# Performance work log

Measured on AMD Instinct MI355X. Metric: run time of the kernel, lower is better.

## Reference

```python
import jax, jax.numpy as jnp
import numpy as np

N_NODES = 50000
N_EDGES = 1600000
F_IN = 256
HID = 256
HEADS = 8
HD = HID // HEADS  # 32
SLOPE = 0.2
EPS = 1e-5


def setup_inputs() -> dict:
    key = jax.random.key(0)
    ks = jax.random.split(key, 10)
    node_features = jax.random.normal(ks[0], (N_NODES, F_IN), jnp.float32)
    edge_index = jax.random.randint(ks[1], (2, N_EDGES), 0, N_NODES, jnp.int32)
    s = 1.0 / np.sqrt(F_IN)
    W = jax.random.uniform(ks[2], (HEADS, F_IN, HD), jnp.float32, -s, s)
    bw = jax.random.uniform(ks[3], (HEADS, HD), jnp.float32, -s, s)
    sa = 1.0 / np.sqrt(2 * HD)
    A = jax.random.uniform(ks[4], (HEADS, 2 * HD), jnp.float32, -sa, sa)
    ba = jax.random.uniform(ks[5], (HEADS,), jnp.float32, -sa, sa)
    gamma = jnp.ones((HEADS, HD), jnp.float32)
    beta = jnp.zeros((HEADS, HD), jnp.float32)
    so = 1.0 / np.sqrt(HD)
    Wout = jax.random.uniform(ks[6], (HD, HID), jnp.float32, -so, so)
    bout = jax.random.uniform(ks[7], (HID,), jnp.float32, -so, so)
    return dict(node_features=node_features, edge_index=edge_index, W=W, bw=bw,
                A=A, ba=ba, gamma=gamma, beta=beta, Wout=Wout, bout=bout)


def _head(x, W, bw, a, ba, gamma, beta, tgt, src):
    h = x @ W + bw                         # [N, d]
    # attn(concat(h_i, h_j)) = h_i @ a1 + h_j @ a2 + ba  (linear over concat)
    si = h @ a[:HD]                        # [N]
    sj = h @ a[HD:]                        # [N]
    e = si[tgt] + sj[src] + ba             # [E]
    e = jnp.where(e >= 0, e, SLOPE * e)    # leaky_relu
    # scatter_softmax over edges grouped by target node (stable)
    m = jax.ops.segment_max(e, tgt, num_segments=N_NODES)
    ex = jnp.exp(e - m[tgt])
    den = jax.ops.segment_sum(ex, tgt, num_segments=N_NODES)
    alpha = ex / den[tgt]                  # [E]  (dropout in eval mode = identity)
    msg = alpha[:, None] * h[src]          # [E, d]
    agg = jax.ops.segment_sum(msg, tgt, num_segments=N_NODES)  # [N, d]
    out = agg + h                          # skip connection
    out = jnp.where(out > 0, out, jnp.expm1(out))  # ELU
    mu = out.mean(axis=-1, keepdims=True)
    var = out.var(axis=-1, keepdims=True)
    return (out - mu) * jax.lax.rsqrt(var + EPS) * gamma + beta


def reference(node_features, edge_index, W, bw, A, ba, gamma, beta, Wout, bout):
    tgt = edge_index[0]
    src = edge_index[1]
    heads = jax.vmap(_head, in_axes=(None, 0, 0, 0, 0, 0, 0, None, None))(
        node_features, W, bw, A, ba, gamma, beta, tgt, src)   # [H, N, d]
    mean = heads.mean(axis=0)                                  # [N, d]
    y = mean @ Wout + bout                                     # [N, HID]
    return jnp.where(y > 0, y, jnp.expm1(y))                   # ELU
```

## Files before the change

kernel.cpp:

```cpp
#include <hip/hip_runtime.h>
#include <hip/hip_bf16.h>

#define N_NODES 50000
#define N_EDGES 1600000
#define HEADS 8
#define HD 32
#define FIN 256
#define HID 256

typedef unsigned short u16;
typedef unsigned int u32;

typedef short s8v __attribute__((ext_vector_type(8)));
typedef float f4v __attribute__((ext_vector_type(4)));

__device__ __forceinline__ float bf2f(u16 v) {
  union { u32 u; float f; } c; c.u = ((u32)v) << 16; return c.f;
}
__device__ __forceinline__ u16 f2bf(float f) {
  union { u32 u; float f; } c; c.f = f;
  u32 u = c.u;
  return (u16)((u + 0x7FFFu + ((u >> 16) & 1u)) >> 16);
}
__device__ __forceinline__ u32 pk2(float lo, float hi) {
  return (u32)f2bf(lo) | ((u32)f2bf(hi) << 16);
}

__global__ __launch_bounds__(256) void k_gemm(
    const float* __restrict__ X, const float* __restrict__ W,
    const float* __restrict__ bw, const float* __restrict__ A,
    u16* __restrict__ Hb, float* __restrict__ si, float* __restrict__ sj) {
  __shared__ __align__(16) u16 Xs[128 * 40];
  __shared__ __align__(16) u16 Wt[128 * 40];

  const int t = threadIdx.x;
  const int m0 = (blockIdx.x >> 1) * 128;
  const int n0 = (blockIdx.x & 1) * 128;
  const int w = t >> 6;
  const int lane = t & 63;
  const int l15 = lane & 15;
  const int quad = lane >> 4;
  const int wm = (w >> 1) * 64;
  const int wn = (w & 1) * 64;

  f4v acc[4][4];
#pragma unroll
  for (int i = 0; i < 4; i++)
#pragma unroll
    for (int j = 0; j < 4; j++) acc[i][j] = (f4v){0.f, 0.f, 0.f, 0.f};

  const int nl = t & 127;
  const int half = t >> 7;
  const int gn = n0 + nl;
  const int gh = gn >> 5, gd = gn & 31;

  for (int k0 = 0; k0 < FIN; k0 += 32) {
#pragma unroll
    for (int p = 0; p < 4; p++) {
      int row = p * 32 + (t >> 3);
      int f4 = t & 7;
      int node = m0 + row;
      float4 xv = make_float4(0.f, 0.f, 0.f, 0.f);
      if (node < N_NODES) xv = *(const float4*)&X[node * FIN + k0 + f4 * 4];
      u32* dst = (u32*)&Xs[row * 40 + f4 * 4];
      dst[0] = pk2(xv.x, xv.y);
      dst[1] = pk2(xv.z, xv.w);
    }
    {
      const float* wp = W + gh * (FIN * HD) + (k0 + half * 16) * HD + gd;
#pragma unroll
      for (int j = 0; j < 8; j++) {
        float lo = wp[(2 * j) * HD];
        float hi = wp[(2 * j + 1) * HD];
        *(u32*)&Wt[nl * 40 + half * 16 + 2 * j] = pk2(lo, hi);
      }
    }
    __syncthreads();
    s8v af[4], bf[4];
#pragma unroll
    for (int mi = 0; mi < 4; mi++)
      af[mi] = *(const s8v*)&Xs[(wm + mi * 16 + l15) * 40 + quad * 8];
#pragma unroll
    for (int ni = 0; ni < 4; ni++)
      bf[ni] = *(const s8v*)&Wt[(wn + ni * 16 + l15) * 40 + quad * 8];
#pragma unroll
    for (int mi = 0; mi < 4; mi++)
#pragma unroll
      for (int ni = 0; ni < 4; ni++)
        acc[mi][ni] = __builtin_amdgcn_mfma_f32_16x16x32_bf16(af[mi], bf[ni], acc[mi][ni], 0, 0, 0);
    __syncthreads();
  }

  const int head0 = (n0 + wn) >> 5;
  const int head1 = head0 + 1;
  float c1a0 = A[head0 * 64 + l15],      c1a1 = A[head0 * 64 + 16 + l15];
  float c2a0 = A[head0 * 64 + 32 + l15], c2a1 = A[head0 * 64 + 48 + l15];
  float c1b0 = A[head1 * 64 + l15],      c1b1 = A[head1 * 64 + 16 + l15];
  float c2b0 = A[head1 * 64 + 32 + l15], c2b1 = A[head1 * 64 + 48 + l15];

#pragma unroll
  for (int mi = 0; mi < 4; mi++) {
#pragma unroll
    for (int ni = 0; ni < 4; ni++) {
      float b = bw[n0 + wn + ni * 16 + l15];
#pragma unroll
      for (int r = 0; r < 4; r++) acc[mi][ni][r] += b;
    }
    const int rbase = m0 + wm + mi * 16 + quad * 4;
#pragma unroll
    for (int r = 0; r < 4; r++) {
      int node = rbase + r;
      if (node < N_NODES) {
#pragma unroll
        for (int ni = 0; ni < 4; ni++) {
          int col = n0 + wn + ni * 16 + l15;
          Hb[node * HID + col] = f2bf(acc[mi][ni][r]);
        }
      }
    }
    float s1a[4], s2a[4], s1b[4], s2b[4];
#pragma unroll
    for (int r = 0; r < 4; r++) {
      s1a[r] = acc[mi][0][r] * c1a0 + acc[mi][1][r] * c1a1;
      s2a[r] = acc[mi][0][r] * c2a0 + acc[mi][1][r] * c2a1;
      s1b[r] = acc[mi][2][r] * c1b0 + acc[mi][3][r] * c1b1;
      s2b[r] = acc[mi][2][r] * c2b0 + acc[mi][3][r] * c2b1;
    }
#pragma unroll
    for (int off = 1; off <= 8; off <<= 1) {
#pragma unroll
      for (int r = 0; r < 4; r++) {
        s1a[r] += __shfl_xor(s1a[r], off);
        s2a[r] += __shfl_xor(s2a[r], off);
        s1b[r] += __shfl_xor(s1b[r], off);
        s2b[r] += __shfl_xor(s2b[r], off);
      }
    }
    if (l15 == 0) {
#pragma unroll
      for (int r = 0; r < 4; r++) {
        int node = rbase + r;
        if (node < N_NODES) {
          si[node * HEADS + head0] = s1a[r];
          sj[node * HEADS + head0] = s2a[r];
          si[node * HEADS + head1] = s1b[r];
          sj[node * HEADS + head1] = s2b[r];
        }
      }
    }
  }
}

__global__ void k_hist(const int* __restrict__ tgt, int* __restrict__ cnt) {
  int e = blockIdx.x * 256 + threadIdx.x;
  if (e < N_EDGES) atomicAdd(&cnt[tgt[e]], 1);
}

__global__ __launch_bounds__(256) void k_scan1(const int* __restrict__ cnt,
    int* __restrict__ excl, int* __restrict__ bsum) {
  __shared__ int s[256];
  const int t = threadIdx.x;
  const int i = blockIdx.x * 256 + t;
  int v = (i < N_NODES) ? cnt[i] : 0;
  s[t] = v;
  __syncthreads();
  int x = v;
  for (int off = 1; off < 256; off <<= 1) {
    int y = (t >= off) ? s[t - off] : 0;
    __syncthreads();
    x += y;
    s[t] = x;
    __syncthreads();
  }
  if (i < N_NODES) excl[i] = x - v;
  if (t == 255) bsum[blockIdx.x] = x;
}

__global__ __launch_bounds__(256) void k_scan2(const int* __restrict__ bsum,
                                               int* __restrict__ boff) {
  __shared__ int s[256];
  const int t = threadIdx.x;
  int v = (t < 196) ? bsum[t] : 0;
  s[t] = v;
  __syncthreads();
  int x = v;
  for (int off = 1; off < 256; off <<= 1) {
    int y = (t >= off) ? s[t - off] : 0;
    __syncthreads();
    x += y;
    s[t] = x;
    __syncthreads();
  }
  if (t < 196) boff[t] = x - v;
}

__global__ void k_scan3(const int* __restrict__ excl, const int* __restrict__ boff,
                        int* __restrict__ rowptr, int* __restrict__ cursor) {
  int i = blockIdx.x * 256 + threadIdx.x;
  if (i < N_NODES) {
    int v = excl[i] + boff[blockIdx.x];
    rowptr[i] = v;
    cursor[i] = v;
  }
}

__global__ void k_scatter(const int* __restrict__ tgt, const int* __restrict__ src,
                          int* __restrict__ cursor, int* __restrict__ sortedSrc) {
  int e = blockIdx.x * 256 + threadIdx.x;
  if (e < N_EDGES) {
    int tg = tgt[e];
    int pos = atomicAdd(&cursor[tg], 1);
    sortedSrc[pos] = src[e];
  }
}

__global__ __launch_bounds__(256) void k_fused(
    const u16* __restrict__ Hb, const float* __restrict__ si,
    const float* __restrict__ sj, const float* __restrict__ ba,
    const float* __restrict__ gamma, const float* __restrict__ beta,
    const float* __restrict__ Wout, const float* __restrict__ bout,
    const int* __restrict__ rowptr, const int* __restrict__ cnt,
    const int* __restrict__ sortedSrc, float* __restrict__ out) {
  __shared__ float exs[32 * 8];
  __shared__ u32   soff[32];
  __shared__ float sbase[8];
  __shared__ float accs[8][256];
  __shared__ float dens[8][32];
  __shared__ float lnorm[256];
  __shared__ float meanv[32];

  const int n = blockIdx.x;
  const int t = threadIdx.x;
  const int cg = t & 31;
  const int es = t >> 5;
  const int hh = cg >> 2;
  const int start = rowptr[n];
  const int deg = cnt[n];
  if (t < 8) sbase[t] = si[n * HEADS + t] + ba[t];
  __syncthreads();

  const int i2c = t >> 3, h8 = t & 7;
  float acc[8] = {0.f, 0.f, 0.f, 0.f, 0.f, 0.f, 0.f, 0.f};
  float den = 0.f;
  for (int base = 0; base < deg; base += 32) {
    const int m = min(32, deg - base);
    {
      float exv = 0.f;
      u32 off0 = 0;
      if (i2c < m) {
        int s = sortedSrc[start + base + i2c];
        float e = sbase[h8] + sj[s * HEADS + h8];
        e = (e >= 0.f) ? e : 0.2f * e;
        exv = __expf(e);
        off0 = (u32)s * (HID * 2);
      }
      exs[i2c * 8 + h8] = exv;
      if (h8 == 0) soff[i2c] = off0;
    }
    __syncthreads();
#pragma unroll
    for (int k = 0; k < 4; k++) {
      int i2 = k * 8 + es;
      u32 off = soff[i2];
      float exv = exs[i2 * 8 + hh];
      float4 hb4 = *(const float4*)((const char*)Hb + off + 16 * cg);
      const u32* hw = (const u32*)&hb4;
#pragma unroll
      for (int d = 0; d < 4; d++) {
        union { u32 u; float f; } lo, hi;
        lo.u = hw[d] << 16;
        hi.u = hw[d] & 0xFFFF0000u;
        acc[2 * d]     += exv * lo.f;
        acc[2 * d + 1] += exv * hi.f;
      }
      den += exv;
    }
    __syncthreads();
  }
#pragma unroll
  for (int j = 0; j < 8; j++) accs[es][cg * 8 + j] = acc[j];
  dens[es][cg] = den;
  __syncthreads();

  float accT = 0.f, denT = 0.f;
#pragma unroll
  for (int e2 = 0; e2 < 8; e2++) {
    accT += accs[e2][t];
    denT += dens[e2][t >> 3];
  }
  float hs = bf2f(Hb[n * HID + t]);
  float v = ((deg > 0) ? (accT / denT) : 0.f) + hs;
  v = (v > 0.f) ? v : expm1f(v);
  float sum = v, sq = v * v;
#pragma unroll
  for (int off = 16; off >= 1; off >>= 1) {
    sum += __shfl_xor(sum, off);
    sq  += __shfl_xor(sq, off);
  }
  float mu = sum * (1.f / 32.f);
  float var = sq * (1.f / 32.f) - mu * mu;
  float nv = (v - mu) * rsqrtf(var + 1e-5f) * gamma[t] + beta[t];
  lnorm[t] = nv;
  __syncthreads();
  if (t < 32) {
    float m2 = 0.f;
#pragma unroll
    for (int h2 = 0; h2 < HEADS; h2++) m2 += lnorm[h2 * 32 + t];
    meanv[t] = m2 * 0.125f;
  }
  __syncthreads();
  float y = bout[t];
#pragma unroll
  for (int k = 0; k < 32; k++) y += meanv[k] * Wout[k * HID + t];
  y = (y > 0.f) ? y : expm1f(y);
  out[n * HID + t] = y;
}

extern "C" void kernel_launch(void* const* d_in, const int* in_sizes, int n_in,
                              void* d_out, int out_size, void* d_ws, size_t ws_size,
                              hipStream_t stream) {
  const float* X     = (const float*)d_in[0];
  const int*   EI    = (const int*)d_in[1];
  const float* W     = (const float*)d_in[2];
  const float* bw    = (const float*)d_in[3];
  const float* A     = (const float*)d_in[4];
  const float* ba    = (const float*)d_in[5];
  const float* gamma = (const float*)d_in[6];
  const float* beta  = (const float*)d_in[7];
  const float* Wout  = (const float*)d_in[8];
  const float* bout  = (const float*)d_in[9];
  float* out = (float*)d_out;
  const int* tgt = EI;
  const int* src = EI + N_EDGES;

  char* ws = (char*)d_ws;
  size_t off = 0;
  auto alloc = [&](size_t bytes) -> void* {
    void* p = ws + off;
    off += bytes;
    off = (off + 255) & ~(size_t)255;
    return p;
  };
  u16*   Hb        = (u16*)  alloc((size_t)N_NODES * HID * 2);
  float* si        = (float*)alloc((size_t)N_NODES * HEADS * 4);
  float* sj        = (float*)alloc((size_t)N_NODES * HEADS * 4);
  int*   cnt       = (int*)  alloc((size_t)N_NODES * 4);
  int*   excl      = (int*)  alloc((size_t)N_NODES * 4);
  int*   bsum      = (int*)  alloc(256 * 4);
  int*   boff      = (int*)  alloc(256 * 4);
  int*   rowptr    = (int*)  alloc((size_t)N_NODES * 4);
  int*   cursor    = (int*)  alloc((size_t)N_NODES * 4);
  int*   sortedSrc = (int*)  alloc((size_t)N_EDGES * 4);

  hipMemsetAsync(cnt, 0, (size_t)N_NODES * 4, stream);
  k_hist<<<(N_EDGES + 255) / 256, 256, 0, stream>>>(tgt, cnt);
  k_scan1<<<196, 256, 0, stream>>>(cnt, excl, bsum);
  k_scan2<<<1, 256, 0, stream>>>(bsum, boff);
  k_scan3<<<196, 256, 0, stream>>>(excl, boff, rowptr, cursor);
  k_scatter<<<(N_EDGES + 255) / 256, 256, 0, stream>>>(tgt, src, cursor, sortedSrc);
  k_gemm<<<((N_NODES + 127) / 128) * 2, 256, 0, stream>>>(X, W, bw, A, Hb, si, sj);
  k_fused<<<N_NODES, 256, 0, stream>>>(Hb, si, sj, ba, gamma, beta, Wout, bout,
                                       rowptr, cnt, sortedSrc, out);
}
```

Before: 526.7 us.

## Gather neighbor features in fp8 and pre-transpose W to bf16

```diff
diff --git a/kernel.cpp b/kernel.cpp
--- a/kernel.cpp
+++ b/kernel.cpp
@@ -10,9 +10,11 @@
 
 typedef unsigned short u16;
 typedef unsigned int u32;
+typedef unsigned char u8;
 
 typedef short s8v __attribute__((ext_vector_type(8)));
 typedef float f4v __attribute__((ext_vector_type(4)));
+typedef float f2v __attribute__((ext_vector_type(2)));
 
 __device__ __forceinline__ float bf2f(u16 v) {
   union { u32 u; float f; } c; c.u = ((u32)v) << 16; return c.f;
@@ -26,8 +28,22 @@
   return (u32)f2bf(lo) | ((u32)f2bf(hi) << 16);
 }
 
+__global__ __launch_bounds__(256) void k_wprep(const float* __restrict__ W,
+                                               u16* __restrict__ Wt_g) {
+  int idx = blockIdx.x * 256 + threadIdx.x;
+  int d4 = idx & 7;
+  int hk = idx >> 3;
+  int h = hk >> 8, k = hk & 255;
+  float4 w = *(const float4*)&W[hk * 32 + d4 * 4];
+  int colb = h * 32 + d4 * 4;
+  Wt_g[(colb + 0) * 256 + k] = f2bf(w.x);
+  Wt_g[(colb + 1) * 256 + k] = f2bf(w.y);
+  Wt_g[(colb + 2) * 256 + k] = f2bf(w.z);
+  Wt_g[(colb + 3) * 256 + k] = f2bf(w.w);
+}
+
 __global__ __launch_bounds__(256) void k_gemm(
-    const float* __restrict__ X, const float* __restrict__ W,
+    const float* __restrict__ X, const u16* __restrict__ Wt_g,
     const float* __restrict__ bw, const float* __restrict__ A,
     u16* __restrict__ Hb, float* __restrict__ si, float* __restrict__ sj) {
   __shared__ __align__(16) u16 Xs[128 * 40];
@@ -51,8 +67,6 @@
 
   const int nl = t & 127;
   const int half = t >> 7;
-  const int gn = n0 + nl;
-  const int gh = gn >> 5, gd = gn & 31;
 
   for (int k0 = 0; k0 < FIN; k0 += 32) {
 #pragma unroll
@@ -67,13 +81,9 @@
       dst[1] = pk2(xv.z, xv.w);
     }
     {
-      const float* wp = W + gh * (FIN * HD) + (k0 + half * 16) * HD + gd;
-#pragma unroll
-      for (int j = 0; j < 8; j++) {
-        float lo = wp[(2 * j) * HD];
-        float hi = wp[(2 * j + 1) * HD];
-        *(u32*)&Wt[nl * 40 + half * 16 + 2 * j] = pk2(lo, hi);
-      }
+      const u16* wp = Wt_g + (n0 + nl) * 256 + k0 + half * 16;
+      *(s8v*)&Wt[nl * 40 + half * 16]     = *(const s8v*)wp;
+      *(s8v*)&Wt[nl * 40 + half * 16 + 8] = *(const s8v*)(wp + 8);
     }
     __syncthreads();
     s8v af[4], bf[4];
@@ -151,6 +161,23 @@
   }
 }
 
+__global__ __launch_bounds__(256) void k_cvt(const u16* __restrict__ Hb,
+                                             u8* __restrict__ Hq) {
+  int idx = blockIdx.x * 256 + threadIdx.x;
+  const u32* p = (const u32*)Hb + (size_t)idx * 4;
+  u32 w0 = p[0], w1 = p[1], w2 = p[2], w3 = p[3];
+  float f0 = bf2f((u16)w0), f1 = bf2f((u16)(w0 >> 16));
+  float f2 = bf2f((u16)w1), f3 = bf2f((u16)(w1 >> 16));
+  float f4 = bf2f((u16)w2), f5 = bf2f((u16)(w2 >> 16));
+  float f6 = bf2f((u16)w3), f7 = bf2f((u16)(w3 >> 16));
+  u32 qa = __builtin_amdgcn_cvt_pk_fp8_f32(f0, f1, 0, false);
+  qa = __builtin_amdgcn_cvt_pk_fp8_f32(f2, f3, qa, true);
+  u32 qb = __builtin_amdgcn_cvt_pk_fp8_f32(f4, f5, 0, false);
+  qb = __builtin_amdgcn_cvt_pk_fp8_f32(f6, f7, qb, true);
+  u32* q = (u32*)Hq + (size_t)idx * 2;
+  q[0] = qa; q[1] = qb;
+}
+
 __global__ void k_hist(const int* __restrict__ tgt, int* __restrict__ cnt) {
   int e = blockIdx.x * 256 + threadIdx.x;
   if (e < N_EDGES) atomicAdd(&cnt[tgt[e]], 1);
@@ -215,32 +242,35 @@
 }
 
 __global__ __launch_bounds__(256) void k_fused(
-    const u16* __restrict__ Hb, const float* __restrict__ si,
-    const float* __restrict__ sj, const float* __restrict__ ba,
-    const float* __restrict__ gamma, const float* __restrict__ beta,
-    const float* __restrict__ Wout, const float* __restrict__ bout,
-    const int* __restrict__ rowptr, const int* __restrict__ cnt,
-    const int* __restrict__ sortedSrc, float* __restrict__ out) {
+    const u8* __restrict__ Hq, const u16* __restrict__ Hb,
+    const float* __restrict__ si, const float* __restrict__ sj,
+    const float* __restrict__ ba, const float* __restrict__ gamma,
+    const float* __restrict__ beta, const float* __restrict__ Wout,
+    const float* __restrict__ bout, const int* __restrict__ rowptr,
+    const int* __restrict__ cnt, const int* __restrict__ sortedSrc,
+    float* __restrict__ out) {
   __shared__ float exs[32 * 8];
   __shared__ u32   soff[32];
   __shared__ float sbase[8];
-  __shared__ float accs[8][256];
-  __shared__ float dens[8][32];
+  __shared__ float accs[16][256];
+  __shared__ float dens[16][16];
   __shared__ float lnorm[256];
   __shared__ float meanv[32];
 
   const int n = blockIdx.x;
   const int t = threadIdx.x;
-  const int cg = t & 31;
-  const int es = t >> 5;
-  const int hh = cg >> 2;
+  const int cg = t & 15;
+  const int es = t >> 4;
+  const int hh = cg >> 1;
   const int start = rowptr[n];
   const int deg = cnt[n];
   if (t < 8) sbase[t] = si[n * HEADS + t] + ba[t];
   __syncthreads();
 
   const int i2c = t >> 3, h8 = t & 7;
-  float acc[8] = {0.f, 0.f, 0.f, 0.f, 0.f, 0.f, 0.f, 0.f};
+  float acc[16];
+#pragma unroll
+  for (int j = 0; j < 16; j++) acc[j] = 0.f;
   float den = 0.f;
   for (int base = 0; base < deg; base += 32) {
     const int m = min(32, deg - base);
@@ -252,41 +282,44 @@
         float e = sbase[h8] + sj[s * HEADS + h8];
         e = (e >= 0.f) ? e : 0.2f * e;
         exv = __expf(e);
-        off0 = (u32)s * (HID * 2);
+        off0 = (u32)s * 256u;
       }
       exs[i2c * 8 + h8] = exv;
       if (h8 == 0) soff[i2c] = off0;
     }
     __syncthreads();
 #pragma unroll
-    for (int k = 0; k < 4; k++) {
-      int i2 = k * 8 + es;
+    for (int k = 0; k < 2; k++) {
+      int i2 = k * 16 + es;
       u32 off = soff[i2];
       float exv = exs[i2 * 8 + hh];
-      float4 hb4 = *(const float4*)((const char*)Hb + off + 16 * cg);
-      const u32* hw = (const u32*)&hb4;
+      float4 q4 = *(const float4*)(Hq + off + 16 * cg);
+      const u32* qw = (const u32*)&q4;
 #pragma unroll
       for (int d = 0; d < 4; d++) {
-        union { u32 u; float f; } lo, hi;
-        lo.u = hw[d] << 16;
-        hi.u = hw[d] & 0xFFFF0000u;
-        acc[2 * d]     += exv * lo.f;
-        acc[2 * d + 1] += exv * hi.f;
+        f2v lo = __builtin_amdgcn_cvt_pk_f32_fp8(qw[d], false);
+        f2v hi = __builtin_amdgcn_cvt_pk_f32_fp8(qw[d], true);
+        acc[4 * d + 0] += exv * lo.x;
+        acc[4 * d + 1] += exv * lo.y;
+        acc[4 * d + 2] += exv * hi.x;
+        acc[4 * d + 3] += exv * hi.y;
       }
       den += exv;
     }
     __syncthreads();
   }
 #pragma unroll
-  for (int j = 0; j < 8; j++) accs[es][cg * 8 + j] = acc[j];
+  for (int j = 0; j < 16; j++)
+    accs[es][cg * 16 + ((j + 2 * cg + es) & 15)] = acc[j];
   dens[es][cg] = den;
   __syncthreads();
 
+  const int cgq = t >> 4, jq = t & 15;
   float accT = 0.f, denT = 0.f;
 #pragma unroll
-  for (int e2 = 0; e2 < 8; e2++) {
-    accT += accs[e2][t];
-    denT += dens[e2][t >> 3];
+  for (int e2 = 0; e2 < 16; e2++) {
+    accT += accs[e2][cgq * 16 + ((jq + 2 * cgq + e2) & 15)];
+    denT += dens[e2][cgq];
   }
   float hs = bf2f(Hb[n * HID + t]);
   float v = ((deg > 0) ? (accT / denT) : 0.f) + hs;
@@ -342,6 +375,8 @@
     return p;
   };
   u16*   Hb        = (u16*)  alloc((size_t)N_NODES * HID * 2);
+  u8*    Hq        = (u8*)   alloc((size_t)N_NODES * HID);
+  u16*   Wt_g      = (u16*)  alloc((size_t)HID * FIN * 2);
   float* si        = (float*)alloc((size_t)N_NODES * HEADS * 4);
   float* sj        = (float*)alloc((size_t)N_NODES * HEADS * 4);
   int*   cnt       = (int*)  alloc((size_t)N_NODES * 4);
@@ -358,7 +393,9 @@
   k_scan2<<<1, 256, 0, stream>>>(bsum, boff);
   k_scan3<<<196, 256, 0, stream>>>(excl, boff, rowptr, cursor);
   k_scatter<<<(N_EDGES + 255) / 256, 256, 0, stream>>>(tgt, src, cursor, sortedSrc);
-  k_gemm<<<((N_NODES + 127) / 128) * 2, 256, 0, stream>>>(X, W, bw, A, Hb, si, sj);
-  k_fused<<<N_NODES, 256, 0, stream>>>(Hb, si, sj, ba, gamma, beta, Wout, bout,
+  k_wprep<<<64, 256, 0, stream>>>(W, Wt_g);
+  k_gemm<<<((N_NODES + 127) / 128) * 2, 256, 0, stream>>>(X, Wt_g, bw, A, Hb, si, sj);
+  k_cvt<<<(N_NODES * HID / 8 + 255) / 256, 256, 0, stream>>>(Hb, Hq);
+  k_fused<<<N_NODES, 256, 0, stream>>>(Hq, Hb, si, sj, ba, gamma, beta, Wout, bout,
                                        rowptr, cnt, sortedSrc, out);
 }
```

After: 540.4 us. 2.6% more time.
